# Kernel optimization log

Measured on AMD Instinct MI355X. Metric: run time of the kernel, lower is better.

Reference implementation:

```python
import jax, jax.numpy as jnp
import numpy as np

B, T, DIM, H, DH = 4, 4096, 1024, 16, 64


def setup_inputs() -> dict:
    key = jax.random.key(0)
    ks = jax.random.split(key, 6)
    s = lambda fan_in: 1.0 / np.sqrt(fan_in)
    x = jax.random.normal(ks[0], (B, T, DIM), dtype=jnp.float32)
    Wq = jax.random.uniform(ks[1], (DIM, H * DH), jnp.float32, -s(DIM), s(DIM))
    Wk = jax.random.uniform(ks[2], (DIM, H * DH), jnp.float32, -s(DIM), s(DIM))
    Wv = jax.random.uniform(ks[3], (DIM, H * DH), jnp.float32, -s(DIM), s(DIM))
    Wo = jax.random.uniform(ks[4], (H * DH, DIM), jnp.float32, -s(H * DH), s(H * DH))
    bo = jax.random.uniform(ks[5], (DIM,), jnp.float32, -s(H * DH), s(H * DH))
    return {"x": x, "Wq": Wq, "Wk": Wk, "Wv": Wv, "Wo": Wo, "bo": bo}


def reference(x, Wq, Wk, Wv, Wo, bo):
    b, t, _ = x.shape
    # projections (no bias, matching nn.Linear(bias=False))
    to_heads = lambda y: y.reshape(b, t, H, DH).transpose(0, 2, 1, 3)  # bhnd
    q = to_heads(x @ Wq)
    k = to_heads(x @ Wk)
    v = to_heads(x @ Wv)
    # linear attention: softmax over feature dim for q, over seq dim for k
    q = jax.nn.softmax(q, axis=-1) * (DH ** -0.5)
    k = jax.nn.softmax(k, axis=-2)
    context = jnp.einsum('bhnd,bhne->bhde', k, v)   # [b,h,dh,dh]
    attn = jnp.einsum('bhnd,bhde->bhne', q, context)  # [b,h,n,dh]
    attn = attn.transpose(0, 2, 1, 3).reshape(b, t, H * DH)
    return attn @ Wo + bo  # dropout is identity at p=0.0 / eval
```

## Files before the change

### kernel.cpp

```cpp
#include <hip/hip_runtime.h>
#include <hip/hip_bf16.h>
#include <cstdint>
#include <cstddef>

#define BB 4
#define TT 4096
#define HH 16
#define NROWS 16384

typedef __attribute__((ext_vector_type(8))) short bf16x8;
typedef __attribute__((ext_vector_type(4))) float f32x4;

__device__ __forceinline__ void gload_lds16(const void* g, void* l) {
  __builtin_amdgcn_global_load_lds(
      (const __attribute__((address_space(1))) void*)g,
      (__attribute__((address_space(3))) void*)l, 16, 0, 0);
}

template <int N>
__device__ __forceinline__ void wait_vmcnt() {
  if constexpr (N == 4)
    asm volatile("s_waitcnt vmcnt(4)" ::: "memory");
  else
    asm volatile("s_waitcnt vmcnt(0)" ::: "memory");
  __builtin_amdgcn_sched_barrier(0);
}

__device__ __forceinline__ void hbar() {
  asm volatile("s_barrier" ::: "memory");
  __builtin_amdgcn_sched_barrier(0);
}

__global__ __launch_bounds__(256) void xconv_k(const float* __restrict__ x,
                                               __hip_bfloat16* __restrict__ xb) {
  const size_t i = ((size_t)blockIdx.x * 256 + threadIdx.x) * 8;
  float4 a = *(const float4*)&x[i];
  float4 b = *(const float4*)&x[i + 4];
  __hip_bfloat16 o[8] __attribute__((aligned(16)));
  o[0] = __float2bfloat16(a.x); o[1] = __float2bfloat16(a.y);
  o[2] = __float2bfloat16(a.z); o[3] = __float2bfloat16(a.w);
  o[4] = __float2bfloat16(b.x); o[5] = __float2bfloat16(b.y);
  o[6] = __float2bfloat16(b.z); o[7] = __float2bfloat16(b.w);
  *(int4*)&xb[i] = *(const int4*)o;
}

__global__ __launch_bounds__(256) void wconv_k(const float* __restrict__ Wq,
                                               const float* __restrict__ Wk,
                                               const float* __restrict__ Wv,
                                               const float* __restrict__ Wo,
                                               __hip_bfloat16* __restrict__ WT) {
  const int which = blockIdx.z;
  const float* W = which == 0 ? Wq : which == 1 ? Wk : which == 2 ? Wv : Wo;
  __shared__ float tile[64][65];
  const int n0 = blockIdx.x * 64, k0 = blockIdx.y * 64;
  const int t = threadIdx.x;
  const int r = t >> 2;
  const int cq = (t & 3) * 16;
#pragma unroll
  for (int i = 0; i < 4; ++i) {
    float4 v = *(const float4*)&W[(size_t)(k0 + r) * 1024 + n0 + cq + i * 4];
    tile[r][cq + i * 4 + 0] = v.x;
    tile[r][cq + i * 4 + 1] = v.y;
    tile[r][cq + i * 4 + 2] = v.z;
    tile[r][cq + i * 4 + 3] = v.w;
  }
  __syncthreads();
  __hip_bfloat16 ob[16] __attribute__((aligned(16)));
#pragma unroll
  for (int j = 0; j < 16; ++j) ob[j] = __float2bfloat16(tile[cq + j][r]);
  __hip_bfloat16* dst = WT + (size_t)(which * 1024 + n0 + r) * 1024 + k0 + cq;
  *(int4*)dst = *(const int4*)&ob[0];
  *(int4*)(dst + 8) = *(const int4*)&ob[8];
}

template <int OMODE, int PB>
__global__ __launch_bounds__(512) void mgemm3_k(
    const __hip_bfloat16* __restrict__ A, int lda,
    const __hip_bfloat16* __restrict__ BT, const float* __restrict__ bias,
    void* __restrict__ Cp, int ldc, int gx) {
  __shared__ __hip_bfloat16 lds[2][32768];

  const int t = threadIdx.x;
  const int wid = t >> 6, l = t & 63;
  const int wr = wid >> 2, wc = wid & 3;

  const int nwg = gridDim.x;
  const int cpx = nwg >> 3;
  const int bid = blockIdx.x;
  const int swz = (bid & 7) * cpx + (bid >> 3);
  const int bx = swz % gx, by = swz / gx;
  const int row0 = by * 256, col0 = bx * 256;

  const __hip_bfloat16* BTb = PB ? BT + ((size_t)(row0 >> 12) << 20) : BT;

  const int sg = l >> 3;
  const int octp = ((l & 7) + sg) & 7;
  const int koct = octp & 3;
  const int srow = 2 * (wid * 16 + sg) + (octp >> 2);
  const __hip_bfloat16* As0 = A + (size_t)(row0 + srow) * lda + koct * 8;
  const __hip_bfloat16* Bs0 = BTb + (size_t)(col0 + srow) * 1024 + koct * 8;

  f32x4 acc[8][4];
#pragma unroll
  for (int m = 0; m < 8; ++m)
#pragma unroll
    for (int n = 0; n < 4; ++n) acc[m][n] = (f32x4){0.f, 0.f, 0.f, 0.f};

  const int lr = l & 15, hk = l >> 4;
  const int slot = (((lr & 1) << 2) + hk - (lr >> 1)) & 7;
  const int rdo = (lr >> 1) * 64 + slot * 8;

  auto stageA = [&](int tn, int c) {
    __hip_bfloat16* d = &lds[tn & 1][c * 8192 + wid * 1024];
    const __hip_bfloat16* s = As0 + tn * 64 + c * 32;
    gload_lds16(s, d);
    gload_lds16(s + (size_t)16 * lda, d + 512);
  };
  auto stageB = [&](int tn, int c) {
    __hip_bfloat16* d = &lds[tn & 1][16384 + c * 8192 + wid * 1024];
    const __hip_bfloat16* s = Bs0 + tn * 64 + c * 32;
    gload_lds16(s, d);
    gload_lds16(s + (size_t)16 * 1024, d + 512);
  };

  stageA(0, 0); stageB(0, 0); stageA(0, 1); stageB(0, 1);

  const __hip_bfloat16* sb = &lds[0][0];
  for (int tn = 0; tn < 16; ++tn) {
    const int bufo = (tn & 1) * 32768;
    const bool pre = tn < 15;
    bf16x8 bfv[4], afv[4];

    wait_vmcnt<4>();
    hbar();
    if (pre) stageA(tn + 1, 0);
#pragma unroll
    for (int n = 0; n < 4; ++n)
      bfv[n] = *(const bf16x8*)(sb + bufo + 16384 + wc * 2048 + n * 512 + rdo);
#pragma unroll
    for (int j = 0; j < 4; ++j)
      afv[j] = *(const bf16x8*)(sb + bufo + wr * 4096 + j * 512 + rdo);
    __builtin_amdgcn_s_setprio(1);
#pragma unroll
    for (int j = 0; j < 4; ++j)
#pragma unroll
      for (int n = 0; n < 4; ++n)
        acc[j][n] = __builtin_amdgcn_mfma_f32_16x16x32_bf16(afv[j], bfv[n],
                                                            acc[j][n], 0, 0, 0);
    __builtin_amdgcn_s_setprio(0);
    if (pre) stageB(tn + 1, 0);
#pragma unroll
    for (int j = 0; j < 4; ++j)
      afv[j] = *(const bf16x8*)(sb + bufo + wr * 4096 + 2048 + j * 512 + rdo);
    __builtin_amdgcn_s_setprio(1);
#pragma unroll
    for (int j = 0; j < 4; ++j)
#pragma unroll
      for (int n = 0; n < 4; ++n)
        acc[4 + j][n] = __builtin_amdgcn_mfma_f32_16x16x32_bf16(
            afv[j], bfv[n], acc[4 + j][n], 0, 0, 0);
    __builtin_amdgcn_s_setprio(0);

    if (pre)
      wait_vmcnt<4>();
    else
      wait_vmcnt<0>();
    hbar();
    if (pre) stageA(tn + 1, 1);
#pragma unroll
    for (int n = 0; n < 4; ++n)
      bfv[n] = *(const bf16x8*)(sb + bufo + 8192 + 16384 + wc * 2048 +
                                n * 512 + rdo);
#pragma unroll
    for (int j = 0; j < 4; ++j)
      afv[j] = *(const bf16x8*)(sb + bufo + 8192 + wr * 4096 + j * 512 + rdo);
    __builtin_amdgcn_s_setprio(1);
#pragma unroll
    for (int j = 0; j < 4; ++j)
#pragma unroll
      for (int n = 0; n < 4; ++n)
        acc[j][n] = __builtin_amdgcn_mfma_f32_16x16x32_bf16(afv[j], bfv[n],
                                                            acc[j][n], 0, 0, 0);
    __builtin_amdgcn_s_setprio(0);
    if (pre) stageB(tn + 1, 1);
#pragma unroll
    for (int j = 0; j < 4; ++j)
      afv[j] = *(const bf16x8*)(sb + bufo + 8192 + wr * 4096 + 2048 + j * 512 +
                                rdo);
    __builtin_amdgcn_s_setprio(1);
#pragma unroll
    for (int j = 0; j < 4; ++j)
#pragma unroll
      for (int n = 0; n < 4; ++n)
        acc[4 + j][n] = __builtin_amdgcn_mfma_f32_16x16x32_bf16(
            afv[j], bfv[n], acc[4 + j][n], 0, 0, 0);
    __builtin_amdgcn_s_setprio(0);
  }

  const int cr = hk * 4;
  const int cc = lr;
  if constexpr (OMODE == 0) {
    __hip_bfloat16* C = (__hip_bfloat16*)Cp;
#pragma unroll
    for (int m = 0; m < 8; ++m)
#pragma unroll
      for (int n = 0; n < 4; ++n) {
        const size_t cb = (size_t)(row0 + wr * 128 + m * 16 + cr) * ldc +
                          col0 + wc * 64 + n * 16 + cc;
#pragma unroll
        for (int j = 0; j < 4; ++j)
          C[cb + (size_t)j * ldc] = __float2bfloat16(acc[m][n][j]);
      }
  } else {
    float* C = (float*)Cp;
    float bv[4];
#pragma unroll
    for (int n = 0; n < 4; ++n) bv[n] = bias[col0 + wc * 64 + n * 16 + cc];
#pragma unroll
    for (int m = 0; m < 8; ++m)
#pragma unroll
      for (int n = 0; n < 4; ++n) {
        const size_t cb = (size_t)(row0 + wr * 128 + m * 16 + cr) * ldc +
                          col0 + wc * 64 + n * 16 + cc;
#pragma unroll
        for (int j = 0; j < 4; ++j)
          C[cb + (size_t)j * ldc] = acc[m][n][j] + bv[n];
      }
  }
}

__global__ __launch_bounds__(256) void ctxkvq_k(__hip_bfloat16* __restrict__ qkv,
                                                float* __restrict__ part,
                                                float* __restrict__ den) {
  __shared__ __hip_bfloat16 ldsb[2 * 8736];
  __hip_bfloat16* ekT = ldsb;
  __hip_bfloat16* vfT = ldsb + 8736;

  const int bh = blockIdx.x;
  const int sc = blockIdx.y;
  const int b = bh >> 4;
  const int h = bh & 15;
  const int t = threadIdx.x;

  const int rr = t >> 1;
  const int c0 = (t & 1) * 32;
  const int w = t >> 6, l = t & 63;
  const int lr = l & 15, hk = l >> 4;
  const int arow = w * 16 + lr;
  const int abase = arow * 136 + ((arow >> 5) & 1) * 32 + hk * 8;

  f32x4 acc[4];
#pragma unroll
  for (int n = 0; n < 4; ++n) acc[n] = (f32x4){0.f, 0.f, 0.f, 0.f};
  float denacc = 0.f;
  const int dd = t >> 2;
  const int dbase = dd * 136 + ((dd >> 5) & 1) * 32;

  for (int c = 0; c < 4; ++c) {
    const int n0 = sc * 512 + c * 128;
    const size_t base =
        (size_t)(b * TT + n0 + rr) * 3072 + 1024 + h * 64 + c0;
    int4 kq[4], vq[4];
#pragma unroll
    for (int i = 0; i < 4; ++i) {
      kq[i] = *(const int4*)(qkv + base + i * 8);
      vq[i] = *(const int4*)(qkv + base + 1024 + i * 8);
    }

    {
      const int g8 = t >> 3;
      const int lc = (t & 7) * 8;
#pragma unroll
      for (int it = 0; it < 4; ++it) {
        const int r = it * 32 + g8;
        __hip_bfloat16* p =
            qkv + (size_t)(b * TT + n0 + r) * 3072 + h * 64 + lc;
        int4 raw = *(const int4*)p;
        const __hip_bfloat16* bp = (const __hip_bfloat16*)&raw;
        float v[8];
        float m = -1e30f;
#pragma unroll
        for (int j = 0; j < 8; ++j) {
          v[j] = __bfloat162float(bp[j]);
          m = fmaxf(m, v[j]);
        }
        m = fmaxf(m, __shfl_xor(m, 1));
        m = fmaxf(m, __shfl_xor(m, 2));
        m = fmaxf(m, __shfl_xor(m, 4));
        float sm = 0.f;
#pragma unroll
        for (int j = 0; j < 8; ++j) {
          v[j] = __expf(v[j] - m);
          sm += v[j];
        }
        sm += __shfl_xor(sm, 1);
        sm += __shfl_xor(sm, 2);
        sm += __shfl_xor(sm, 4);
        const float inv = 0.125f / sm;
        __hip_bfloat16 o[8] __attribute__((aligned(16)));
#pragma unroll
        for (int j = 0; j < 8; ++j) o[j] = __float2bfloat16(v[j] * inv);
        *(int4*)p = *(const int4*)o;
      }
    }

    __syncthreads();
#pragma unroll
    for (int i = 0; i < 4; ++i) {
      const __hip_bfloat16* kp = (const __hip_bfloat16*)&kq[i];
      const __hip_bfloat16* vp = (const __hip_bfloat16*)&vq[i];
#pragma unroll
      for (int j = 0; j < 8; ++j) {
        const int cidx = c0 + i * 8 + j;
        const int off = cidx * 136 + ((cidx >> 5) & 1) * 32 + rr;
        ekT[off] = __float2bfloat16(__expf(__bfloat162float(kp[j])));
        vfT[off] = vp[j];
      }
    }
    __syncthreads();

#pragma unroll
    for (int ks = 0; ks < 4; ++ks) {
      bf16x8 af = *(const bf16x8*)(ekT + abase + ks * 32);
#pragma unroll
      for (int n = 0; n < 4; ++n) {
        const int brow = n * 16 + lr;
        bf16x8 bf = *(const bf16x8*)(vfT + brow * 136 +
                                     ((brow >> 5) & 1) * 32 + hk * 8 + ks * 32);
        acc[n] =
            __builtin_amdgcn_mfma_f32_16x16x32_bf16(af, bf, acc[n], 0, 0, 0);
      }
    }

    if ((t & 3) == 0) {
#pragma unroll
      for (int q8 = 0; q8 < 16; ++q8) {
        bf16x8 e8 = *(const bf16x8*)(ekT + dbase + q8 * 8);
        const __hip_bfloat16* ep = (const __hip_bfloat16*)&e8;
#pragma unroll
        for (int j = 0; j < 8; ++j) denacc += __bfloat162float(ep[j]);
      }
    }
  }

  float* pb = part + ((size_t)bh * 8 + sc) * 4096;
#pragma unroll
  for (int n = 0; n < 4; ++n)
#pragma unroll
    for (int j = 0; j < 4; ++j)
      pb[(w * 16 + hk * 4 + j) * 64 + n * 16 + lr] = acc[n][j];

  if ((t & 3) == 0) den[((size_t)bh * 8 + sc) * 64 + dd] = denacc;
}

__global__ __launch_bounds__(256) void ctx_reduce_k(
    const float* __restrict__ part, const float* __restrict__ den,
    __hip_bfloat16* __restrict__ ctxb) {
  const int bh = blockIdx.x, q = blockIdx.y, t = threadIdx.x;
  const int idx = q * 1024 + t * 4;
  const int d = idx >> 6;
  float sden = 0.f;
  for (int s = 0; s < 8; ++s) sden += den[((size_t)bh * 8 + s) * 64 + d];
  float4 sv = {0.f, 0.f, 0.f, 0.f};
  const float* pb = part + (size_t)bh * 8 * 4096 + idx;
  for (int s = 0; s < 8; ++s) {
    float4 v = *(const float4*)(pb + (size_t)s * 4096);
    sv.x += v.x; sv.y += v.y; sv.z += v.z; sv.w += v.w;
  }
  const float di = 1.0f / sden;
  __hip_bfloat16 ob[4] __attribute__((aligned(8)));
  ob[0] = __float2bfloat16(sv.x * di);
  ob[1] = __float2bfloat16(sv.y * di);
  ob[2] = __float2bfloat16(sv.z * di);
  ob[3] = __float2bfloat16(sv.w * di);
  *(int2*)&ctxb[(size_t)bh * 4096 + idx] = *(const int2*)ob;
}

__global__ __launch_bounds__(256) void wfuse_k(
    const __hip_bfloat16* __restrict__ WT,
    const __hip_bfloat16* __restrict__ ctxb, __hip_bfloat16* __restrict__ WfT) {
  const int bh = blockIdx.x;
  const int b = bh >> 4, h = bh & 15;
  const int t = threadIdx.x, w = t >> 6, l = t & 63;
  const int n1 = blockIdx.y * 64 + w * 16;
  const int lr = l & 15, hk = l >> 4;

  f32x4 acc[4];
#pragma unroll
  for (int n = 0; n < 4; ++n) acc[n] = (f32x4){0.f, 0.f, 0.f, 0.f};

  const __hip_bfloat16* Abase =
      WT + (size_t)(3072 + n1 + lr) * 1024 + h * 64 + hk * 8;
  const __hip_bfloat16* Bbase = ctxb + (size_t)bh * 4096 + hk * 8;

#pragma unroll
  for (int kk2 = 0; kk2 < 2; ++kk2) {
    bf16x8 af = *(const bf16x8*)(Abase + kk2 * 32);
#pragma unroll
    for (int n = 0; n < 4; ++n) {
      bf16x8 bf = *(const bf16x8*)(Bbase + (n * 16 + lr) * 64 + kk2 * 32);
      acc[n] = __builtin_amdgcn_mfma_f32_16x16x32_bf16(af, bf, acc[n], 0, 0, 0);
    }
  }

  __hip_bfloat16* W0 = WfT + ((size_t)b << 20) + (size_t)(n1 + hk * 4) * 1024 +
                       h * 64 + lr;
#pragma unroll
  for (int n = 0; n < 4; ++n)
#pragma unroll
    for (int j = 0; j < 4; ++j)
      W0[(size_t)j * 1024 + n * 16] = __float2bfloat16(acc[n][j]);
}

extern "C" void kernel_launch(void* const* d_in, const int* in_sizes, int n_in,
                              void* d_out, int out_size, void* d_ws,
                              size_t ws_size, hipStream_t stream) {
  const float* x = (const float*)d_in[0];
  const float* Wq = (const float*)d_in[1];
  const float* Wk = (const float*)d_in[2];
  const float* Wv = (const float*)d_in[3];
  const float* Wo = (const float*)d_in[4];
  const float* bo = (const float*)d_in[5];
  float* out = (float*)d_out;

  char* ws = (char*)d_ws;
  __hip_bfloat16* qkv = (__hip_bfloat16*)ws;
  __hip_bfloat16* WT = (__hip_bfloat16*)(ws + 100663296ull);
  float* den = (float*)(ws + 100663296ull + 8388608ull);
  __hip_bfloat16* ctxb =
      (__hip_bfloat16*)(ws + 100663296ull + 8388608ull + 524288ull);
  __hip_bfloat16* WfT =
      (__hip_bfloat16*)(ws + 100663296ull + 8388608ull + 1048576ull);
  __hip_bfloat16* xb = (__hip_bfloat16*)d_out;
  float* part = (float*)((char*)d_out + 33554432ull);

  const dim3 blk(256);

  xconv_k<<<dim3(NROWS * 1024 / 8 / 256), blk, 0, stream>>>(x, xb);
  wconv_k<<<dim3(16, 16, 4), blk, 0, stream>>>(Wq, Wk, Wv, Wo, WT);

  mgemm3_k<0, 0><<<dim3(768), dim3(512), 0, stream>>>(xb, 1024, WT, nullptr,
                                                      qkv, 3072, 12);

  ctxkvq_k<<<dim3(64, 8), blk, 0, stream>>>(qkv, part, den);
  ctx_reduce_k<<<dim3(64, 4), blk, 0, stream>>>(part, den, ctxb);
  wfuse_k<<<dim3(64, 16), blk, 0, stream>>>(WT, ctxb, WfT);

  mgemm3_k<1, 1><<<dim3(256), dim3(512), 0, stream>>>(qkv, 3072, WfT, bo, out,
                                                      1024, 4);
}
```

Measured before the change: 190.2 us.

## Merge conversion kernels and add a smaller-LDS QKV GEMM with K-step of 32

Merges the x-to-bf16 and weight transpose/convert kernels into a single prep kernel, dispatching on block index, which saves one launch. Adds a new QKV projection GEMM (mgemm6) that stages 32-wide K slices into a double-buffered LDS of half the previous size, using 16x16x32 bf16 MFMAs and a per-step barrier. The smaller LDS footprint may let more workgroups share a CU. The trade-off is twice as many K iterations and barriers, each with a full vmcnt(0) wait.

```diff
diff --git a/kernel.cpp b/kernel.cpp
--- a/kernel.cpp
+++ b/kernel.cpp
@@ -31,29 +31,32 @@
   __builtin_amdgcn_sched_barrier(0);
 }
 
-__global__ __launch_bounds__(256) void xconv_k(const float* __restrict__ x,
-                                               __hip_bfloat16* __restrict__ xb) {
-  const size_t i = ((size_t)blockIdx.x * 256 + threadIdx.x) * 8;
-  float4 a = *(const float4*)&x[i];
-  float4 b = *(const float4*)&x[i + 4];
-  __hip_bfloat16 o[8] __attribute__((aligned(16)));
-  o[0] = __float2bfloat16(a.x); o[1] = __float2bfloat16(a.y);
-  o[2] = __float2bfloat16(a.z); o[3] = __float2bfloat16(a.w);
-  o[4] = __float2bfloat16(b.x); o[5] = __float2bfloat16(b.y);
-  o[6] = __float2bfloat16(b.z); o[7] = __float2bfloat16(b.w);
-  *(int4*)&xb[i] = *(const int4*)o;
-}
-
-__global__ __launch_bounds__(256) void wconv_k(const float* __restrict__ Wq,
-                                               const float* __restrict__ Wk,
-                                               const float* __restrict__ Wv,
-                                               const float* __restrict__ Wo,
-                                               __hip_bfloat16* __restrict__ WT) {
-  const int which = blockIdx.z;
+__global__ __launch_bounds__(256) void prep_k(const float* __restrict__ x,
+                                              const float* __restrict__ Wq,
+                                              const float* __restrict__ Wk,
+                                              const float* __restrict__ Wv,
+                                              const float* __restrict__ Wo,
+                                              __hip_bfloat16* __restrict__ xb,
+                                              __hip_bfloat16* __restrict__ WT) {
+  const int t = threadIdx.x;
+  if (blockIdx.x < 8192) {
+    const size_t i = ((size_t)blockIdx.x * 256 + t) * 8;
+    float4 a = *(const float4*)&x[i];
+    float4 b = *(const float4*)&x[i + 4];
+    __hip_bfloat16 o[8] __attribute__((aligned(16)));
+    o[0] = __float2bfloat16(a.x); o[1] = __float2bfloat16(a.y);
+    o[2] = __float2bfloat16(a.z); o[3] = __float2bfloat16(a.w);
+    o[4] = __float2bfloat16(b.x); o[5] = __float2bfloat16(b.y);
+    o[6] = __float2bfloat16(b.z); o[7] = __float2bfloat16(b.w);
+    *(int4*)&xb[i] = *(const int4*)o;
+    return;
+  }
+  const int bid2 = blockIdx.x - 8192;
+  const int which = bid2 >> 8;
+  const int sub = bid2 & 255;
   const float* W = which == 0 ? Wq : which == 1 ? Wk : which == 2 ? Wv : Wo;
   __shared__ float tile[64][65];
-  const int n0 = blockIdx.x * 64, k0 = blockIdx.y * 64;
-  const int t = threadIdx.x;
+  const int n0 = (sub & 15) * 64, k0 = (sub >> 4) * 64;
   const int r = t >> 2;
   const int cq = (t & 3) * 16;
 #pragma unroll
@@ -71,6 +74,124 @@
   __hip_bfloat16* dst = WT + (size_t)(which * 1024 + n0 + r) * 1024 + k0 + cq;
   *(int4*)dst = *(const int4*)&ob[0];
   *(int4*)(dst + 8) = *(const int4*)&ob[8];
+}
+
+template <int OMODE, int PB>
+__global__ __launch_bounds__(512) void mgemm6_k(
+    const __hip_bfloat16* __restrict__ A, int lda,
+    const __hip_bfloat16* __restrict__ BT, const float* __restrict__ bias,
+    void* __restrict__ Cp, int ldc, int gx) {
+  __shared__ __hip_bfloat16 lds[2][16384];
+
+  const int t = threadIdx.x;
+  const int wid = t >> 6, l = t & 63;
+  const int wr = wid >> 2, wc = wid & 3;
+
+  const int nwg = gridDim.x;
+  const int cpx = nwg >> 3;
+  const int bid = blockIdx.x;
+  const int swz = (bid & 7) * cpx + (bid >> 3);
+  const int bx = swz % gx, by = swz / gx;
+  const int row0 = by * 256, col0 = bx * 256;
+
+  const __hip_bfloat16* BTb = PB ? BT + ((size_t)(row0 >> 12) << 20) : BT;
+
+  const int sg = l >> 3;
+  const int octp = ((l & 7) + sg) & 7;
+  const int koct = octp & 3;
+  const int srow = 2 * (wid * 16 + sg) + (octp >> 2);
+  const __hip_bfloat16* As0 = A + (size_t)(row0 + srow) * lda + koct * 8;
+  const __hip_bfloat16* Bs0 = BTb + (size_t)(col0 + srow) * 1024 + koct * 8;
+
+  f32x4 acc[8][4];
+#pragma unroll
+  for (int m = 0; m < 8; ++m)
+#pragma unroll
+    for (int n = 0; n < 4; ++n) acc[m][n] = (f32x4){0.f, 0.f, 0.f, 0.f};
+
+  const int lr = l & 15, hk = l >> 4;
+  const int slot = (((lr & 1) << 2) + hk - (lr >> 1)) & 7;
+  const int rdo = (lr >> 1) * 64 + slot * 8;
+
+  auto stage = [&](int u) {
+    __hip_bfloat16* d = &lds[u & 1][wid * 1024];
+    const __hip_bfloat16* sa = As0 + u * 32;
+    const __hip_bfloat16* sb = Bs0 + u * 32;
+    gload_lds16(sa, d);
+    gload_lds16(sa + (size_t)16 * lda, d + 512);
+    gload_lds16(sb, d + 8192);
+    gload_lds16(sb + (size_t)16 * 1024, d + 8192 + 512);
+  };
+
+  stage(0);
+  wait_vmcnt<0>();
+  hbar();
+
+  for (int u = 0; u < 32; ++u) {
+    if (u < 31) stage(u + 1);
+    const __hip_bfloat16* s = &lds[u & 1][0];
+    bf16x8 bfv[4], afv[4];
+#pragma unroll
+    for (int n = 0; n < 4; ++n)
+      bfv[n] = *(const bf16x8*)(s + 8192 + wc * 2048 + n * 512 + rdo);
+#pragma unroll
+    for (int j = 0; j < 4; ++j)
+      afv[j] = *(const bf16x8*)(s + wr * 4096 + j * 512 + rdo);
+    __builtin_amdgcn_s_setprio(1);
+#pragma unroll
+    for (int j = 0; j < 4; ++j)
+#pragma unroll
+      for (int n = 0; n < 4; ++n)
+        acc[j][n] = __builtin_amdgcn_mfma_f32_16x16x32_bf16(afv[j], bfv[n],
+                                                            acc[j][n], 0, 0, 0);
+    __builtin_amdgcn_s_setprio(0);
+#pragma unroll
+    for (int j = 0; j < 4; ++j)
+      afv[j] = *(const bf16x8*)(s + wr * 4096 + 2048 + j * 512 + rdo);
+    __builtin_amdgcn_s_setprio(1);
+#pragma unroll
+    for (int j = 0; j < 4; ++j)
+#pragma unroll
+      for (int n = 0; n < 4; ++n)
+        acc[4 + j][n] = __builtin_amdgcn_mfma_f32_16x16x32_bf16(
+            afv[j], bfv[n], acc[4 + j][n], 0, 0, 0);
+    __builtin_amdgcn_s_setprio(0);
+    if (u < 31) {
+      wait_vmcnt<0>();
+      hbar();
+    }
+  }
+
+  const int cr = hk * 4;
+  const int cc = lr;
+  if constexpr (OMODE == 0) {
+    __hip_bfloat16* C = (__hip_bfloat16*)Cp;
+#pragma unroll
+    for (int m = 0; m < 8; ++m)
+#pragma unroll
+      for (int n = 0; n < 4; ++n) {
+        const size_t cb = (size_t)(row0 + wr * 128 + m * 16 + cr) * ldc +
+                          col0 + wc * 64 + n * 16 + cc;
+#pragma unroll
+        for (int j = 0; j < 4; ++j)
+          C[cb + (size_t)j * ldc] = __float2bfloat16(acc[m][n][j]);
+      }
+  } else {
+    float* C = (float*)Cp;
+    float bv[4];
+#pragma unroll
+    for (int n = 0; n < 4; ++n) bv[n] = bias[col0 + wc * 64 + n * 16 + cc];
+#pragma unroll
+    for (int m = 0; m < 8; ++m)
+#pragma unroll
+      for (int n = 0; n < 4; ++n) {
+        const size_t cb = (size_t)(row0 + wr * 128 + m * 16 + cr) * ldc +
+                          col0 + wc * 64 + n * 16 + cc;
+#pragma unroll
+        for (int j = 0; j < 4; ++j)
+          C[cb + (size_t)j * ldc] = acc[m][n][j] + bv[n];
+      }
+  }
 }
 
 template <int OMODE, int PB>
@@ -436,10 +557,9 @@
 
   const dim3 blk(256);
 
-  xconv_k<<<dim3(NROWS * 1024 / 8 / 256), blk, 0, stream>>>(x, xb);
-  wconv_k<<<dim3(16, 16, 4), blk, 0, stream>>>(Wq, Wk, Wv, Wo, WT);
-
-  mgemm3_k<0, 0><<<dim3(768), dim3(512), 0, stream>>>(xb, 1024, WT, nullptr,
+  prep_k<<<dim3(9216), blk, 0, stream>>>(x, Wq, Wk, Wv, Wo, xb, WT);
+
+  mgemm6_k<0, 0><<<dim3(768), dim3(512), 0, stream>>>(xb, 1024, WT, nullptr,
                                                       qkv, 3072, 12);
 
   ctxkvq_k<<<dim3(64, 8), blk, 0, stream>>>(qkv, part, den);
```

Result: slower. 196.7 us (+3.5%).
